# Kernel tuning notes

Measured on AMD Instinct MI355X. Metric: run time of the kernel, lower is better.

## Reference

```python
import jax, jax.numpy as jnp
import numpy as np

B = 1048576


def _normalize_rotation_matrix(R):
    # Faithful to torch: U, S, V = svd(R); Rn = U @ V^T; flip whole U by sign(det); recompute.
    U, S, Vh = jnp.linalg.svd(R)  # R = U diag(S) Vh, so torch's V^T == Vh
    Rn = jnp.matmul(U, Vh)
    det = jnp.linalg.det(Rn)[:, None, None]
    sign = jnp.sign(det)
    U = U * sign
    return jnp.matmul(U, Vh)


def _quat_to_rotmat(q):
    # q: [B, 4] as (w, x, y, z); same element layout as the torch loop, vectorized.
    w, x, y, z = q[:, 0], q[:, 1], q[:, 2], q[:, 3]
    R = jnp.stack([
        1 - 2 * (y ** 2 + z ** 2), 2 * (x * y - w * z),     2 * (x * z + w * y),
        2 * (x * y + w * z),       1 - 2 * (x ** 2 + z ** 2), 2 * (y * z - w * x),
        2 * (x * z - w * y),       2 * (y * z + w * x),     1 - 2 * (x ** 2 + y ** 2),
    ], axis=-1)
    return R.reshape(-1, 3, 3)


def setup_inputs() -> dict:
    key = jax.random.key(0)
    k1, k2, k3 = jax.random.split(key, 3)
    pred_R = jax.random.normal(k1, (B, 3, 3), dtype=jnp.float32)
    pred_t = jax.random.normal(k2, (B, 1, 3), dtype=jnp.float32)
    gt_transform = jax.random.normal(k3, (B, 7), dtype=jnp.float32)
    return {"pred_R": pred_R, "pred_t": pred_t, "gt_transform": gt_transform}


def reference(pred_R, pred_t, gt_transform):
    gt_quat = gt_transform[:, :4]
    igt_t = gt_transform[:, 4:]
    igt_R = _quat_to_rotmat(gt_quat)              # [B,3,3]
    igt_R = _normalize_rotation_matrix(igt_R)
    pred_Rn = _normalize_rotation_matrix(pred_R)
    # matmul(pred_R^T, igt_R): [b,i,k] = sum_j pred_Rn[b,j,i] * igt_R[b,j,k]
    M = jnp.einsum('bji,bjk->bik', pred_Rn, igt_R)
    eye = jnp.eye(3, dtype=M.dtype)
    rot_loss = jnp.mean((M - eye) ** 2)
    t_loss = jnp.mean((pred_t - igt_t[:, None, :]) ** 2)
    return rot_loss + t_loss
```

## Files before the change

kernel.cpp:

```cpp
#include <hip/hip_runtime.h>


#define SCALED_ITERS 3
#define PLAIN_ITERS  1

__device__ __forceinline__ float se3_elem(const float* __restrict__ R,
                                          const float* __restrict__ Q,
                                          const float* __restrict__ T)
{
    float w  = Q[0], x = Q[1], y = Q[2], z = Q[3];

    float v2 = x*x + y*y + z*z;
    float c  = 1.0f - 2.0f*v2;
    float r2 = fmaxf(c*c + 4.0f*(w*w)*v2, 1e-30f);
    float rr = __builtin_amdgcn_rsqf(r2);
    float ga = c * rr;
    float gt_ = (1.0f - ga) * __builtin_amdgcn_rcpf(fmaxf(v2, 1e-37f));
    float gb = 2.0f * w * rr;

    float tx = gt_*x, ty = gt_*y, tz = gt_*z;
    float bx = gb*x,  by = gb*y,  bz = gb*z;

    float G0 = ga + tx*x,  G1 = tx*y - bz,   G2 = tx*z + by;
    float G3 = tx*y + bz,  G4 = ga + ty*y,   G5 = ty*z - bx;
    float G6 = tx*z - by,  G7 = ty*z + bx,   G8 = ga + tz*z;

    float X0 = R[0], X1 = R[1], X2 = R[2];
    float X3 = R[3], X4 = R[4], X5 = R[5];
    float X6 = R[6], X7 = R[7], X8 = R[8];

    float s = 1.0f;
#pragma unroll
    for (int it = 0; it < SCALED_ITERS + PLAIN_ITERS; ++it) {
        float C0 = X4*X8 - X5*X7;
        float C1 = X5*X6 - X3*X8;
        float C2 = X3*X7 - X4*X6;
        float C3 = X2*X7 - X1*X8;
        float C4 = X0*X8 - X2*X6;
        float C5 = X1*X6 - X0*X7;
        float C6 = X1*X5 - X2*X4;
        float C7 = X2*X3 - X0*X5;
        float C8 = X0*X4 - X1*X3;
        float det = X0*C0 + X1*C1 + X2*C2;
        if (it == 0) s = (det < 0.0f) ? -1.0f : 1.0f;
        float ka, kb;
        if (it < SCALED_ITERS) {
            float ad = fminf(fmaxf(fabsf(det), 1e-30f), 1e30f);
            float g  = __builtin_amdgcn_exp2f(0.33333333f * __builtin_amdgcn_logf(ad));
            ka = 0.5f * __builtin_amdgcn_rcpf(g);
            kb = 0.5f * g * __builtin_amdgcn_rcpf(det);
        } else {
            ka = 0.5f;
            kb = 0.5f * __builtin_amdgcn_rcpf(det);
        }
        if (it == SCALED_ITERS + PLAIN_ITERS - 1) { ka *= s; kb *= s; }
        X0 = ka*X0 + kb*C0;  X1 = ka*X1 + kb*C1;  X2 = ka*X2 + kb*C2;
        X3 = ka*X3 + kb*C3;  X4 = ka*X4 + kb*C4;  X5 = ka*X5 + kb*C5;
        X6 = ka*X6 + kb*C6;  X7 = ka*X7 + kb*C7;  X8 = ka*X8 + kb*C8;
    }

    float d0 = G0-X0, d1 = G1-X1, d2 = G2-X2;
    float d3 = G3-X3, d4 = G4-X4, d5 = G5-X5;
    float d6 = G6-X6, d7 = G7-X7, d8 = G8-X8;
    float rot = d0*d0 + d1*d1 + d2*d2
              + d3*d3 + d4*d4 + d5*d5
              + d6*d6 + d7*d7 + d8*d8;

    float e0 = T[0] - Q[4];
    float e1 = T[1] - Q[5];
    float e2 = T[2] - Q[6];
    float tl = e0*e0 + e1*e1 + e2*e2;

    return rot * (1.0f/9.0f) + tl * (1.0f/3.0f);
}

__global__ __launch_bounds__(256) void se3_loss_kernel(
    const float* __restrict__ pred_R,
    const float* __restrict__ pred_t,
    const float* __restrict__ gt,
    float* __restrict__ out, int B, float invB)
{
    float acc = 0.0f;
    int t = blockIdx.x * blockDim.x + threadIdx.x;
    if (4*t < B) {
        const float4* rp = reinterpret_cast<const float4*>(pred_R) + t*9;
        const float4* qp = reinterpret_cast<const float4*>(gt)     + t*7;
        const float4* tp = reinterpret_cast<const float4*>(pred_t) + t*3;

        float4 rv[9], qv[7], tv[3];
#pragma unroll
        for (int k = 0; k < 9; ++k) rv[k] = rp[k];
#pragma unroll
        for (int k = 0; k < 7; ++k) qv[k] = qp[k];
#pragma unroll
        for (int k = 0; k < 3; ++k) tv[k] = tp[k];

        float R[36], Q[28], T[12];
#pragma unroll
        for (int k = 0; k < 9; ++k) { R[4*k]=rv[k].x; R[4*k+1]=rv[k].y; R[4*k+2]=rv[k].z; R[4*k+3]=rv[k].w; }
#pragma unroll
        for (int k = 0; k < 7; ++k) { Q[4*k]=qv[k].x; Q[4*k+1]=qv[k].y; Q[4*k+2]=qv[k].z; Q[4*k+3]=qv[k].w; }
#pragma unroll
        for (int k = 0; k < 3; ++k) { T[4*k]=tv[k].x; T[4*k+1]=tv[k].y; T[4*k+2]=tv[k].z; T[4*k+3]=tv[k].w; }

#pragma unroll
        for (int e = 0; e < 4; ++e)
            acc += se3_elem(R + 9*e, Q + 7*e, T + 3*e);
        acc *= invB;
    }

#pragma unroll
    for (int off = 32; off > 0; off >>= 1)
        acc += __shfl_down(acc, off, 64);

    __shared__ float wsums[4];
    int lane = threadIdx.x & 63;
    int wid  = threadIdx.x >> 6;
    if (lane == 0) wsums[wid] = acc;
    __syncthreads();
    if (threadIdx.x == 0) {
        float tot = wsums[0] + wsums[1] + wsums[2] + wsums[3];
        atomicAdd(out, tot);
    }
}

extern "C" void kernel_launch(void* const* d_in, const int* in_sizes, int n_in,
                              void* d_out, int out_size, void* d_ws, size_t ws_size,
                              hipStream_t stream) {
    const float* pred_R = (const float*)d_in[0];
    const float* pred_t = (const float*)d_in[1];
    const float* gt     = (const float*)d_in[2];
    float* out = (float*)d_out;
    int B = in_sizes[0] / 9;

    hipMemsetAsync(out, 0, sizeof(float), stream);

    const int block = 256;
    const int nthreads = (B + 3) / 4;
    const int grid = (nthreads + block - 1) / block;
    se3_loss_kernel<<<grid, block, 0, stream>>>(pred_R, pred_t, gt, out, B,
                                                1.0f / (float)B);
}
```

Measured before the change: 119.2 us.

## Stage inputs through LDS with coalesced loads, one element per thread

Each block now cooperatively copies a 256-element tile of rotations, quaternions and translations into shared memory with contiguous float4 loads, then each thread processes one element from LDS instead of four from registers. This targets uncoalesced strided global loads and high register pressure. In exchange it adds a barrier, LDS traffic, and four times as many blocks and atomic adds.

```diff
diff --git a/kernel.cpp b/kernel.cpp
--- a/kernel.cpp
+++ b/kernel.cpp
@@ -1,6 +1,7 @@
 #include <hip/hip_runtime.h>
 
 
+#define TILE 256
 #define SCALED_ITERS 3
 #define PLAIN_ITERS  1
 
@@ -74,51 +75,63 @@
     return rot * (1.0f/9.0f) + tl * (1.0f/3.0f);
 }
 
-__global__ __launch_bounds__(256) void se3_loss_kernel(
+__global__ __launch_bounds__(256, 8) void se3_loss_kernel(
     const float* __restrict__ pred_R,
     const float* __restrict__ pred_t,
     const float* __restrict__ gt,
     float* __restrict__ out, int B, float invB)
 {
+    __shared__ __align__(16) float ldsR[TILE * 9];
+    __shared__ __align__(16) float ldsQ[TILE * 7];
+    __shared__ __align__(16) float ldsT[TILE * 3];
+    __shared__ float wsums[4];
+
+    const int tid  = threadIdx.x;
+    const int base = blockIdx.x * TILE;
+    int count = B - base;
+    if (count > TILE) count = TILE;
+
+    if (count == TILE) {
+        const float4* sR = reinterpret_cast<const float4*>(pred_R) + (size_t)blockIdx.x * (TILE * 9 / 4);
+        const float4* sQ = reinterpret_cast<const float4*>(gt)     + (size_t)blockIdx.x * (TILE * 7 / 4);
+        const float4* sT = reinterpret_cast<const float4*>(pred_t) + (size_t)blockIdx.x * (TILE * 3 / 4);
+        float4* dR = reinterpret_cast<float4*>(ldsR);
+        float4* dQ = reinterpret_cast<float4*>(ldsQ);
+        float4* dT = reinterpret_cast<float4*>(ldsT);
+
+        float4 r0 = sR[tid];
+        float4 r1 = sR[tid + 256];
+        float4 r2; if (tid < 64)  r2 = sR[tid + 512];
+        float4 q0 = sQ[tid];
+        float4 q1; if (tid < 192) q1 = sQ[tid + 256];
+        float4 t0; if (tid < 192) t0 = sT[tid];
+
+        dR[tid]       = r0;
+        dR[tid + 256] = r1;
+        if (tid < 64)  dR[tid + 512] = r2;
+        dQ[tid]       = q0;
+        if (tid < 192) dQ[tid + 256] = q1;
+        if (tid < 192) dT[tid]       = t0;
+    } else {
+        for (int i = tid; i < count * 9; i += 256) ldsR[i] = pred_R[(size_t)base * 9 + i];
+        for (int i = tid; i < count * 7; i += 256) ldsQ[i] = gt[(size_t)base * 7 + i];
+        for (int i = tid; i < count * 3; i += 256) ldsT[i] = pred_t[(size_t)base * 3 + i];
+    }
+    __syncthreads();
+
     float acc = 0.0f;
-    int t = blockIdx.x * blockDim.x + threadIdx.x;
-    if (4*t < B) {
-        const float4* rp = reinterpret_cast<const float4*>(pred_R) + t*9;
-        const float4* qp = reinterpret_cast<const float4*>(gt)     + t*7;
-        const float4* tp = reinterpret_cast<const float4*>(pred_t) + t*3;
-
-        float4 rv[9], qv[7], tv[3];
-#pragma unroll
-        for (int k = 0; k < 9; ++k) rv[k] = rp[k];
-#pragma unroll
-        for (int k = 0; k < 7; ++k) qv[k] = qp[k];
-#pragma unroll
-        for (int k = 0; k < 3; ++k) tv[k] = tp[k];
-
-        float R[36], Q[28], T[12];
-#pragma unroll
-        for (int k = 0; k < 9; ++k) { R[4*k]=rv[k].x; R[4*k+1]=rv[k].y; R[4*k+2]=rv[k].z; R[4*k+3]=rv[k].w; }
-#pragma unroll
-        for (int k = 0; k < 7; ++k) { Q[4*k]=qv[k].x; Q[4*k+1]=qv[k].y; Q[4*k+2]=qv[k].z; Q[4*k+3]=qv[k].w; }
-#pragma unroll
-        for (int k = 0; k < 3; ++k) { T[4*k]=tv[k].x; T[4*k+1]=tv[k].y; T[4*k+2]=tv[k].z; T[4*k+3]=tv[k].w; }
-
-#pragma unroll
-        for (int e = 0; e < 4; ++e)
-            acc += se3_elem(R + 9*e, Q + 7*e, T + 3*e);
-        acc *= invB;
-    }
+    if (tid < count)
+        acc = se3_elem(&ldsR[9 * tid], &ldsQ[7 * tid], &ldsT[3 * tid]) * invB;
 
 #pragma unroll
     for (int off = 32; off > 0; off >>= 1)
         acc += __shfl_down(acc, off, 64);
 
-    __shared__ float wsums[4];
-    int lane = threadIdx.x & 63;
-    int wid  = threadIdx.x >> 6;
+    int lane = tid & 63;
+    int wid  = tid >> 6;
     if (lane == 0) wsums[wid] = acc;
     __syncthreads();
-    if (threadIdx.x == 0) {
+    if (tid == 0) {
         float tot = wsums[0] + wsums[1] + wsums[2] + wsums[3];
         atomicAdd(out, tot);
     }
@@ -136,8 +149,7 @@
     hipMemsetAsync(out, 0, sizeof(float), stream);
 
     const int block = 256;
-    const int nthreads = (B + 3) / 4;
-    const int grid = (nthreads + block - 1) / block;
+    const int grid  = (B + TILE - 1) / TILE;
     se3_loss_kernel<<<grid, block, 0, stream>>>(pred_R, pred_t, gt, out, B,
                                                 1.0f / (float)B);
 }
```

New measurement: 145.4 us. 21.9% more time.
